# Kernel tuning notes

Measured on AMD Instinct MI355X. Metric: run time of the kernel, lower is better.

## Reference

```python
import jax, jax.numpy as jnp
import numpy as np

B, S, D = 1, 512, 2048
H, KVH, HD = 16, 16, 128          # heads, kv heads, head_dim = D // H
E, K, I = 64, 6, 1408             # routed experts, top_k, moe intermediate
NSH = 2
ISH = NSH * I                     # shared expert intermediate
EPS = 1e-6
THETA = 10000.0
SCALE = HD ** -0.5


def setup_inputs() -> dict:
    key = jax.random.key(0)
    ks = jax.random.split(key, 12)
    s = 0.02
    rn = lambda k, shape: s * jax.random.normal(k, shape, dtype=jnp.float32)
    return {
        "positions": jnp.arange(B * S, dtype=jnp.int32).reshape(B, S),
        "hidden_states": jax.random.normal(ks[0], (B, S, D), dtype=jnp.float32),
        "residual": jax.random.normal(ks[1], (B, S, D), dtype=jnp.float32),
        "ln1_w": jnp.ones((D,), jnp.float32),
        "ln2_w": jnp.ones((D,), jnp.float32),
        "wqkv": rn(ks[2], ((H + 2 * KVH) * HD, D)),
        "wo": rn(ks[3], (D, H * HD)),
        "gate_w": rn(ks[4], (E, D)),
        "w1": rn(ks[5], (E, 2 * I, D)),   # packed gate_up per expert
        "w2": rn(ks[6], (E, D, I)),       # down per expert
        "sw1": rn(ks[7], (2 * ISH, D)),   # shared expert gate_up
        "sw2": rn(ks[8], (D, ISH)),       # shared expert down
    }


def _rmsnorm(x, w):
    var = jnp.mean(x * x, axis=-1, keepdims=True)
    return x * jax.lax.rsqrt(var + EPS) * w


def _rope(x, pos):
    # x: [B, S, n_heads, HD], neox style (rotate halves), full rotary dim
    half = HD // 2
    inv_freq = 1.0 / (THETA ** (jnp.arange(half, dtype=jnp.float32) * 2.0 / HD))
    ang = pos.astype(jnp.float32)[..., None] * inv_freq        # [B, S, half]
    cos = jnp.cos(ang)[:, :, None, :]
    sin = jnp.sin(ang)[:, :, None, :]
    x1, x2 = jnp.split(x, 2, axis=-1)
    return jnp.concatenate([x1 * cos - x2 * sin, x2 * cos + x1 * sin], axis=-1)


def _swiglu(x, w_gate_up, w_down):
    gu = x @ w_gate_up.T
    g, u = jnp.split(gu, 2, axis=-1)
    return (jax.nn.silu(g) * u) @ w_down.T


def reference(positions, hidden_states, residual, ln1_w, ln2_w, wqkv, wo,
              gate_w, w1, w2, sw1, sw2):
    # --- input_layernorm with fused residual add (vLLM RMSNorm semantics) ---
    x = hidden_states + residual
    residual = x
    h = _rmsnorm(x, ln1_w)

    # --- attention: qkv proj, RoPE, causal attention (prefill), o proj ---
    qkv = h @ wqkv.T                                           # [B, S, (H+2KVH)*HD]
    q, k, v = jnp.split(qkv, [H * HD, (H + KVH) * HD], axis=-1)
    q = q.reshape(B, S, H, HD)
    k = k.reshape(B, S, KVH, HD)
    v = v.reshape(B, S, KVH, HD)
    q = _rope(q, positions)
    k = _rope(k, positions)
    scores = jnp.einsum("bqhd,bkhd->bhqk", q, k) * SCALE
    causal = jnp.tril(jnp.ones((S, S), dtype=bool))
    scores = jnp.where(causal, scores, -jnp.inf)
    attn = jax.nn.softmax(scores, axis=-1)
    ctx = jnp.einsum("bhqk,bkhd->bqhd", attn, v).reshape(B, S, H * HD)
    h = ctx @ wo.T

    # --- post_attention_layernorm with fused residual add ---
    x = h + residual
    residual = x
    h = _rmsnorm(x, ln2_w)

    # --- MoE: shared expert + softmax gate + top-k dispatch ---
    xt = h.reshape(B * S, D)                                   # [T, D]
    T = B * S
    shared = _swiglu(xt, sw1, sw2)                             # [T, D]
    logits = xt @ gate_w.T                                     # [T, E]
    probs = jax.nn.softmax(logits.astype(jnp.float32), axis=-1)
    topw, topi = jax.lax.top_k(probs, K)                       # [T, K]
    # norm_topk_prob = False -> no renormalization
    combine = jnp.zeros((T, E), jnp.float32).at[
        jnp.arange(T)[:, None], topi].add(topw)                # [T, E]

    def expert_step(acc, ew):
        w1e, w2e, ce = ew                                      # [2I,D], [D,I], [T]
        out = _swiglu(xt, w1e, w2e)                            # [T, D]
        return acc + ce[:, None] * out, None

    moe_out, _ = jax.lax.scan(expert_step, jnp.zeros_like(xt),
                              (w1, w2, combine.T))
    out = (moe_out + shared).reshape(B, S, D)
    return out, residual
```

## Files before the change

kernel.cpp:

```cpp
#include <hip/hip_runtime.h>
#include <hip/hip_bf16.h>


typedef __attribute__((ext_vector_type(4))) float  f32x4;
typedef __attribute__((ext_vector_type(8))) short  short8;
typedef __attribute__((ext_vector_type(8))) unsigned short ushort8;

#define SS    512
#define DD    2048
#define NH    16
#define HDIM  128
#define NQKV  6144
#define NEXP  64
#define TOPK  6
#define IEXP  1408
#define ISHE  2816
#define MAXTILE 128
#define ATT_SCALE 0.08838834764831845f

__device__ __forceinline__ float u2f(unsigned short u) {
  return __uint_as_float(((unsigned int)u) << 16);
}
__device__ __forceinline__ unsigned short f2u(float f) {
  __hip_bfloat16 h = __float2bfloat16(f);
  return *reinterpret_cast<unsigned short*>(&h);
}
__device__ __forceinline__ ushort8 cvt8(f32x4 a, f32x4 b) {
  ushort8 r;
  r[0]=f2u(a[0]); r[1]=f2u(a[1]); r[2]=f2u(a[2]); r[3]=f2u(a[3]);
  r[4]=f2u(b[0]); r[5]=f2u(b[1]); r[6]=f2u(b[2]); r[7]=f2u(b[3]);
  return r;
}

__global__ __launch_bounds__(256) void addnorm1_k(
    const float* __restrict__ hid, const float* __restrict__ res,
    const float* __restrict__ w, float* __restrict__ x1,
    unsigned short* __restrict__ h1)
{
  int t = blockIdx.x, tid = threadIdx.x;
  long long base = (long long)t * DD + tid * 8;
  float x[8]; float ss = 0.f;
#pragma unroll
  for (int i = 0; i < 8; i++) {
    x[i] = hid[base + i] + res[base + i];
    ss += x[i] * x[i]; x1[base + i] = x[i];
  }
#pragma unroll
  for (int o = 1; o < 64; o <<= 1) ss += __shfl_xor(ss, o);
  __shared__ float r4[4];
  if ((tid & 63) == 0) r4[tid >> 6] = ss;
  __syncthreads();
  ss = r4[0] + r4[1] + r4[2] + r4[3];
  float rr = rsqrtf(ss * (1.f / DD) + 1e-6f);
#pragma unroll
  for (int i = 0; i < 8; i++) h1[base + i] = f2u(x[i] * rr * w[tid * 8 + i]);
}

__global__ __launch_bounds__(256) void addnorm2_k(
    const unsigned short* __restrict__ attn, const float* __restrict__ x1,
    const float* __restrict__ w, float* __restrict__ resid_out,
    unsigned short* __restrict__ h3)
{
  int t = blockIdx.x, tid = threadIdx.x;
  long long base = (long long)t * DD + tid * 8;
  ushort8 va = *(const ushort8*)(attn + base);
  float x[8]; float ss = 0.f;
#pragma unroll
  for (int i = 0; i < 8; i++) {
    x[i] = u2f(va[i]) + x1[base + i]; ss += x[i] * x[i];
    resid_out[base + i] = x[i];
  }
#pragma unroll
  for (int o = 1; o < 64; o <<= 1) ss += __shfl_xor(ss, o);
  __shared__ float r4[4];
  if ((tid & 63) == 0) r4[tid >> 6] = ss;
  __syncthreads();
  ss = r4[0] + r4[1] + r4[2] + r4[3];
  float rr = rsqrtf(ss * (1.f / DD) + 1e-6f);
#pragma unroll
  for (int i = 0; i < 8; i++) h3[base + i] = f2u(x[i] * rr * w[tid * 8 + i]);
}

template<int BN>
__global__ __launch_bounds__(256) void gemm_dense(
    const unsigned short* __restrict__ A, const float* __restrict__ W,
    unsigned short* __restrict__ C, int Nh, int K, int lda, int Mdense)
{
  constexpr int WN  = BN / 2;
  constexpr int NF  = WN / 16;
  constexpr int TPR = 256 / BN;
  constexpr int FPT = BN / 4;
  constexpr int NV  = FPT / 4;
  __shared__ __align__(16) unsigned short As[64][72];
  __shared__ __align__(16) unsigned short Bg[BN][72];

  int m0 = blockIdx.y * 64, cnt = Mdense;
  int n0 = blockIdx.x * BN;
  int tid = threadIdx.x;
  int sr  = tid >> 2;
  int sce = (tid & 3) * 16;
  int sr2 = tid / TPR;
  int sc2 = (tid % TPR) * FPT;

  int am = m0 + sr; if (am >= cnt) am = cnt - 1;
  const unsigned short* ap = A + (long long)am * lda + sce;
  const float* gp = W + (long long)(n0 + sr2) * K + sc2;

  int lane = tid & 63, w = tid >> 6;
  int wm = (w >> 1) * 32, wn = (w & 1) * WN;
  int l15 = lane & 15, hi = lane >> 4;

  f32x4 acc[2][NF] = {};
  ushort8 ra0, ra1;
  f32x4 rg[NV];

  ra0 = *(const ushort8*)(ap);
  ra1 = *(const ushort8*)(ap + 8);
#pragma unroll
  for (int i = 0; i < NV; i++) rg[i] = *(const f32x4*)(gp + 4 * i);

  for (int k0 = 0; k0 < K; k0 += 64) {
    __syncthreads();
    *(ushort8*)&As[sr][sce]     = ra0;
    *(ushort8*)&As[sr][sce + 8] = ra1;
#pragma unroll
    for (int i = 0; i < NV / 2; i++)
      *(ushort8*)&Bg[sr2][sc2 + i * 8] = cvt8(rg[2 * i], rg[2 * i + 1]);
    __syncthreads();
    if (k0 + 64 < K) {
      ra0 = *(const ushort8*)(ap + k0 + 64);
      ra1 = *(const ushort8*)(ap + k0 + 72);
#pragma unroll
      for (int i = 0; i < NV; i++) rg[i] = *(const f32x4*)(gp + k0 + 64 + 4 * i);
    }
#pragma unroll
    for (int kk = 0; kk < 2; kk++) {
      int kc = kk * 32 + hi * 8;
      short8 fa[2], fg[NF];
#pragma unroll
      for (int f = 0; f < 2; f++) fa[f] = *(const short8*)&As[wm + f * 16 + l15][kc];
#pragma unroll
      for (int f = 0; f < NF; f++) fg[f] = *(const short8*)&Bg[wn + f * 16 + l15][kc];
#pragma unroll
      for (int fm = 0; fm < 2; fm++)
#pragma unroll
        for (int fn = 0; fn < NF; fn++)
          acc[fm][fn] = __builtin_amdgcn_mfma_f32_16x16x32_bf16(fa[fm], fg[fn], acc[fm][fn], 0, 0, 0);
    }
  }

  int r0q = hi * 4;
#pragma unroll
  for (int fm = 0; fm < 2; fm++) {
#pragma unroll
    for (int j = 0; j < 4; j++) {
      int m = m0 + wm + fm * 16 + r0q + j;
      if (m >= cnt) continue;
      unsigned short* Cp = C + (long long)m * Nh + n0 + wn;
#pragma unroll
      for (int fn = 0; fn < NF; fn++)
        Cp[fn * 16 + l15] = f2u(acc[fm][fn][j]);
    }
  }
}

template<int STAGE>
__global__ __launch_bounds__(256) void moe_k(
    const unsigned short* __restrict__ h3,
    const unsigned short* __restrict__ act_e_in, const unsigned short* __restrict__ act_sh_in,
    const float* __restrict__ w1, const float* __restrict__ sw1,
    const float* __restrict__ w2, const float* __restrict__ sw2,
    unsigned short* __restrict__ act_e_out, unsigned short* __restrict__ act_sh_out,
    unsigned short* __restrict__ out_e, unsigned short* __restrict__ shared_o,
    const int* __restrict__ e_cnt, const int* __restrict__ e_off,
    const int* __restrict__ tok_list, const float* __restrict__ wslot,
    const int* __restrict__ tile_tab, const int* __restrict__ ntiles)
{
  constexpr bool SILU = (STAGE == 0);
  __shared__ __align__(16) unsigned short As[64][72];
  __shared__ __align__(16) unsigned short Bg[64][72];
  __shared__ __align__(16) unsigned short Bu[SILU ? 64 : 1][72];

  int y = blockIdx.y;
  if (y >= *ntiles) return;
  int tt = tile_tab[y];
  int e = tt >> 8;
  int m0 = (tt & 255) * 64;
  bool sh = (e == NEXP);
  int cnt  = sh ? SS : e_cnt[e];
  int roff = sh ? 0 : e_off[e];
  int n0 = blockIdx.x * 64;

  int Nh, K, lda;
  const float* Wb;
  const unsigned short* Abase;
  unsigned short* Cb;
  if (STAGE == 0) {
    K = DD; lda = DD; Abase = h3;
    if (sh) { Nh = ISHE; Wb = sw1; Cb = act_sh_out; }
    else    { Nh = IEXP; Wb = w1 + (long long)e * 2 * IEXP * DD; Cb = act_e_out; }
    if (n0 >= Nh) return;
  } else {
    Nh = DD;
    if (sh) { K = ISHE; lda = ISHE; Abase = act_sh_in; Wb = sw2; Cb = shared_o; }
    else    { K = IEXP; lda = IEXP; Abase = act_e_in;
              Wb = w2 + (long long)e * DD * IEXP; Cb = out_e; }
  }

  int tid = threadIdx.x;
  int sr  = tid >> 2;
  int sce = (tid & 3) * 16;

  int am = m0 + sr; if (am >= cnt) am = cnt - 1;
  int arow;
  if (STAGE == 0) arow = sh ? am : tok_list[roff + am];
  else            arow = sh ? am : roff + am;
  const unsigned short* ap = Abase + (long long)arow * lda + sce;
  const float* gp = Wb + (long long)(n0 + sr) * K + sce;
  const float* up = SILU ? (Wb + (long long)(Nh + n0 + sr) * K + sce) : nullptr;

  int lane = tid & 63, wid = tid >> 6;
  int wm = (wid >> 1) * 32, wn = (wid & 1) * 32;
  int l15 = lane & 15, hi = lane >> 4;

  f32x4 acc[2][2] = {};
  f32x4 accU[2][2] = {};
  ushort8 raA0, raA1, raB0, raB1;
  f32x4 rgA[4], ruA[4], rgB[4], ruB[4];

#define MLOAD(k, r0, r1, g, u)                                     \
  do {                                                             \
    r0 = *(const ushort8*)(ap + (k));                              \
    r1 = *(const ushort8*)(ap + (k) + 8);                          \
    _Pragma("unroll")                                              \
    for (int i_ = 0; i_ < 4; i_++) g[i_] = *(const f32x4*)(gp + (k) + 4 * i_); \
    if (SILU) {                                                    \
      _Pragma("unroll")                                            \
      for (int i_ = 0; i_ < 4; i_++) u[i_] = *(const f32x4*)(up + (k) + 4 * i_); \
    }                                                              \
  } while (0)

#define MSTORE(r0, r1, g, u)                                       \
  do {                                                             \
    *(ushort8*)&As[sr][sce]     = r0;                              \
    *(ushort8*)&As[sr][sce + 8] = r1;                              \
    *(ushort8*)&Bg[sr][sce]     = cvt8(g[0], g[1]);                \
    *(ushort8*)&Bg[sr][sce + 8] = cvt8(g[2], g[3]);                \
    if (SILU) {                                                    \
      *(ushort8*)&Bu[sr][sce]     = cvt8(u[0], u[1]);              \
      *(ushort8*)&Bu[sr][sce + 8] = cvt8(u[2], u[3]);              \
    }                                                              \
  } while (0)

#define MMFMA                                                      \
  do {                                                             \
    _Pragma("unroll")                                              \
    for (int kk = 0; kk < 2; kk++) {                               \
      int kc = kk * 32 + hi * 8;                                   \
      short8 fa[2], fg[2];                                         \
      _Pragma("unroll")                                            \
      for (int f = 0; f < 2; f++) {                                \
        fa[f] = *(const short8*)&As[wm + f * 16 + l15][kc];        \
        fg[f] = *(const short8*)&Bg[wn + f * 16 + l15][kc];        \
      }                                                            \
      _Pragma("unroll")                                            \
      for (int fm = 0; fm < 2; fm++)                               \
        _Pragma("unroll")                                          \
        for (int fn = 0; fn < 2; fn++)                             \
          acc[fm][fn] = __builtin_amdgcn_mfma_f32_16x16x32_bf16(fa[fm], fg[fn], acc[fm][fn], 0, 0, 0); \
      if (SILU) {                                                  \
        short8 fu[2];                                              \
        _Pragma("unroll")                                          \
        for (int f = 0; f < 2; f++) fu[f] = *(const short8*)&Bu[wn + f * 16 + l15][kc]; \
        _Pragma("unroll")                                          \
        for (int fm = 0; fm < 2; fm++)                             \
          _Pragma("unroll")                                        \
          for (int fn = 0; fn < 2; fn++)                           \
            accU[fm][fn] = __builtin_amdgcn_mfma_f32_16x16x32_bf16(fa[fm], fu[fn], accU[fm][fn], 0, 0, 0); \
      }                                                            \
    }                                                              \
  } while (0)

  MLOAD(0,  raA0, raA1, rgA, ruA);
  MLOAD(64, raB0, raB1, rgB, ruB);
  for (int k0 = 0; k0 < K; k0 += 128) {
    __syncthreads();
    MSTORE(raA0, raA1, rgA, ruA);
    __syncthreads();
    if (k0 + 128 < K) MLOAD(k0 + 128, raA0, raA1, rgA, ruA);
    MMFMA;
    __syncthreads();
    MSTORE(raB0, raB1, rgB, ruB);
    __syncthreads();
    if (k0 + 192 < K) MLOAD(k0 + 192, raB0, raB1, rgB, ruB);
    MMFMA;
  }
#undef MLOAD
#undef MSTORE
#undef MMFMA

  int r0q = hi * 4;
#pragma unroll
  for (int fm = 0; fm < 2; fm++) {
#pragma unroll
    for (int j = 0; j < 4; j++) {
      int m = m0 + wm + fm * 16 + r0q + j;
      if (m >= cnt) continue;
      long long crow = sh ? m : (roff + m);
      float scale = (STAGE == 1 && !sh) ? wslot[crow] : 1.f;
      unsigned short* Cp = Cb + crow * (long long)Nh + n0 + wn;
#pragma unroll
      for (int fn = 0; fn < 2; fn++) {
        float v;
        if (SILU) {
          float g = acc[fm][fn][j], u = accU[fm][fn][j];
          v = (g / (1.f + __expf(-g))) * u;
        } else v = acc[fm][fn][j];
        Cp[fn * 16 + l15] = f2u(v * scale);
      }
    }
  }
}

__global__ __launch_bounds__(256) void rope_k(
    const int* __restrict__ pos, const unsigned short* __restrict__ qkv,
    unsigned short* __restrict__ qr, unsigned short* __restrict__ kr)
{
  int t = blockIdx.x, tid = threadIdx.x;
  __shared__ float cs[64], sn[64];
  if (tid < 64) {
    float inv = __expf(-((float)(2 * tid) / 128.f) * logf(10000.f));
    float ang = (float)pos[t] * inv;
    cs[tid] = cosf(ang); sn[tid] = sinf(ang);
  }
  __syncthreads();
  const unsigned short* row = qkv + (long long)t * NQKV;
  for (int idx = tid; idx < NH * 64; idx += 256) {
    int hh = idx >> 6, i = idx & 63;
    long long o = ((long long)hh * SS + t) * HDIM;
    float x1 = u2f(row[hh*128 + i]), x2 = u2f(row[hh*128 + i + 64]);
    qr[o + i]      = f2u(x1 * cs[i] - x2 * sn[i]);
    qr[o + i + 64] = f2u(x2 * cs[i] + x1 * sn[i]);
    float y1 = u2f(row[2048 + hh*128 + i]), y2 = u2f(row[2048 + hh*128 + i + 64]);
    kr[o + i]      = f2u(y1 * cs[i] - y2 * sn[i]);
    kr[o + i + 64] = f2u(y2 * cs[i] + y1 * sn[i]);
  }
}

__global__ __launch_bounds__(256) void attn_k(
    const unsigned short* __restrict__ qr, const unsigned short* __restrict__ kr,
    const unsigned short* __restrict__ qkv, unsigned short* __restrict__ ctx)
{
  int h = blockIdx.x, qt = blockIdx.y, q0 = qt * 64;
  int tid = threadIdx.x, lane = tid & 63, w = tid >> 6;
  int l15 = lane & 15, hi = lane >> 4;

  __shared__ unsigned short Vt[128][72];
  __shared__ unsigned short Pl[4][16][72];

  short8 qf[4];
  const unsigned short* Qb = qr + ((long long)h * SS + q0 + w * 16 + l15) * HDIM + hi * 8;
#pragma unroll
  for (int kf = 0; kf < 4; kf++) qf[kf] = *(const short8*)(Qb + kf * 32);

  f32x4 o[8] = {};
  float m_run[4] = {-1e30f, -1e30f, -1e30f, -1e30f};
  float l_run[4] = {};
  int myq = w * 16 + hi * 4;

  int ntile = qt + 1;
  for (int kt = 0; kt < ntile; kt++) {
    int kbase = kt * 64;
    __syncthreads();
    {
      int r = lane, d0 = w * 32;
      const unsigned short* Vp = qkv + (long long)(kbase + r) * NQKV + 4096 + h * HDIM + d0;
#pragma unroll
      for (int c = 0; c < 4; c++) {
        ushort8 v = *(const ushort8*)(Vp + c * 8);
#pragma unroll
        for (int i = 0; i < 8; i++) Vt[d0 + c * 8 + i][r] = v[i];
      }
    }
    f32x4 s[4] = {};
    const unsigned short* Kb = kr + ((long long)h * SS + kbase) * HDIM + hi * 8;
#pragma unroll
    for (int nf = 0; nf < 4; nf++) {
      const unsigned short* Kp = Kb + (long long)(nf * 16 + l15) * HDIM;
#pragma unroll
      for (int kf = 0; kf < 4; kf++) {
        short8 kf8 = *(const short8*)(Kp + kf * 32);
        s[nf] = __builtin_amdgcn_mfma_f32_16x16x32_bf16(qf[kf], kf8, s[nf], 0, 0, 0);
      }
    }
    bool diag = (kt == qt);
#pragma unroll
    for (int nf = 0; nf < 4; nf++) {
      int keyl = nf * 16 + l15;
#pragma unroll
      for (int j = 0; j < 4; j++) {
        float sv = s[nf][j] * ATT_SCALE;
        if (diag && keyl > myq + j) sv = -1e30f;
        s[nf][j] = sv;
      }
    }
    float corr[4], mnew[4];
#pragma unroll
    for (int j = 0; j < 4; j++) {
      float mv = fmaxf(fmaxf(s[0][j], s[1][j]), fmaxf(s[2][j], s[3][j]));
#pragma unroll
      for (int ox = 1; ox < 16; ox <<= 1) mv = fmaxf(mv, __shfl_xor(mv, ox));
      mnew[j] = fmaxf(m_run[j], mv);
      corr[j] = __expf(m_run[j] - mnew[j]);
      m_run[j] = mnew[j];
    }
#pragma unroll
    for (int nf8 = 0; nf8 < 8; nf8++)
#pragma unroll
      for (int j = 0; j < 4; j++) o[nf8][j] *= corr[j];
    float rs[4] = {};
#pragma unroll
    for (int nf = 0; nf < 4; nf++) {
#pragma unroll
      for (int j = 0; j < 4; j++) {
        float pv = __expf(s[nf][j] - mnew[j]);
        rs[j] += pv;
        Pl[w][hi * 4 + j][nf * 16 + l15] = f2u(pv);
      }
    }
#pragma unroll
    for (int j = 0; j < 4; j++) {
      float sv = rs[j];
#pragma unroll
      for (int ox = 1; ox < 16; ox <<= 1) sv += __shfl_xor(sv, ox);
      l_run[j] = l_run[j] * corr[j] + sv;
    }
    __syncthreads();
#pragma unroll
    for (int kf2 = 0; kf2 < 2; kf2++) {
      short8 pa = *(const short8*)&Pl[w][l15][kf2 * 32 + hi * 8];
#pragma unroll
      for (int nf8 = 0; nf8 < 8; nf8++) {
        short8 vb = *(const short8*)&Vt[nf8 * 16 + l15][kf2 * 32 + hi * 8];
        o[nf8] = __builtin_amdgcn_mfma_f32_16x16x32_bf16(pa, vb, o[nf8], 0, 0, 0);
      }
    }
  }
#pragma unroll
  for (int j = 0; j < 4; j++) {
    float inv = 1.f / l_run[j];
    long long t = q0 + myq + j;
    unsigned short* Cp = ctx + t * (long long)DD + h * HDIM;
#pragma unroll
    for (int nf8 = 0; nf8 < 8; nf8++)
      Cp[nf8 * 16 + l15] = f2u(o[nf8][j] * inv);
  }
}

__global__ __launch_bounds__(256) void gating_k(
    const unsigned short* __restrict__ h3, const float* __restrict__ gw,
    int* __restrict__ topi, float* __restrict__ topw)
{
  int b = blockIdx.x, tid = threadIdx.x;
  int e = tid & 63, g = tid >> 6;
  __shared__ float p[8][NEXP];
  const float* wr = gw + (long long)e * DD;
  int t0 = b * 8 + g * 2;
  const unsigned short* h0 = h3 + (long long)t0 * DD;
  const unsigned short* h1 = h0 + DD;
  float a0 = 0.f, a1 = 0.f;
  for (int k = 0; k < DD; k += 8) {
    f32x4 w0 = *(const f32x4*)(wr + k);
    f32x4 w1 = *(const f32x4*)(wr + k + 4);
    ushort8 x0 = *(const ushort8*)(h0 + k);
    ushort8 x1 = *(const ushort8*)(h1 + k);
    a0 += u2f(x0[0])*w0[0] + u2f(x0[1])*w0[1] + u2f(x0[2])*w0[2] + u2f(x0[3])*w0[3]
        + u2f(x0[4])*w1[0] + u2f(x0[5])*w1[1] + u2f(x0[6])*w1[2] + u2f(x0[7])*w1[3];
    a1 += u2f(x1[0])*w0[0] + u2f(x1[1])*w0[1] + u2f(x1[2])*w0[2] + u2f(x1[3])*w0[3]
        + u2f(x1[4])*w1[0] + u2f(x1[5])*w1[1] + u2f(x1[6])*w1[2] + u2f(x1[7])*w1[3];
  }
  p[g * 2][e] = a0; p[g * 2 + 1][e] = a1;
  __syncthreads();
  if (tid < 8) {
    int t = b * 8 + tid;
    float* pr = p[tid];
    float mx = -1e30f;
    for (int j = 0; j < NEXP; j++) mx = fmaxf(mx, pr[j]);
    float s = 0.f;
    for (int j = 0; j < NEXP; j++) { pr[j] = __expf(pr[j] - mx); s += pr[j]; }
    float invs = 1.f / s;
    for (int j = 0; j < NEXP; j++) pr[j] *= invs;
    for (int r = 0; r < TOPK; r++) {
      int bi = 0; float bv = -1.f;
      for (int j = 0; j < NEXP; j++) if (pr[j] > bv) { bv = pr[j]; bi = j; }
      topi[t * TOPK + r] = bi; topw[t * TOPK + r] = bv; pr[bi] = -2.f;
    }
  }
}

__global__ __launch_bounds__(256) void route_k(
    const int* __restrict__ topi, const float* __restrict__ topw,
    int* __restrict__ ecnt, int* __restrict__ eoff,
    int* __restrict__ tok_list, int* __restrict__ slotg,
    float* __restrict__ wslot, int* __restrict__ tile_tab,
    int* __restrict__ ntiles)
{
  __shared__ int ti[SS * TOPK];
  __shared__ int c4[NEXP][4];
  __shared__ int ctot[NEXP];
  __shared__ int offs[NEXP + 1];
  int tid = threadIdx.x;
  for (int i = tid; i < SS * TOPK; i += 256) ti[i] = topi[i];
  __syncthreads();
  int e = tid >> 2, q = tid & 3;
  const int QW = SS * TOPK / 4;
  int lo = q * QW, hiQ = lo + QW;
  int n = 0;
  for (int i = lo; i < hiQ; i++) n += (ti[i] == e);
  c4[e][q] = n;
  __syncthreads();
  if (q == 0) {
    int s = c4[e][0] + c4[e][1] + c4[e][2] + c4[e][3];
    ctot[e] = s; ecnt[e] = s;
  }
  __syncthreads();
  if (tid == 0) {
    offs[0] = 0;
    for (int k = 0; k < NEXP; k++) offs[k + 1] = offs[k] + ctot[k];
    int nt = 0;
    for (int k = 0; k < NEXP; k++)
      for (int mt = 0; mt * 64 < ctot[k]; mt++) tile_tab[nt++] = (k << 8) | mt;
    for (int mt = 0; mt < SS / 64; mt++) tile_tab[nt++] = (NEXP << 8) | mt;
    *ntiles = nt;
  }
  __syncthreads();
  if (q == 0) eoff[e] = offs[e];
  int idx = offs[e];
  for (int qq = 0; qq < q; qq++) idx += c4[e][qq];
  for (int i = lo; i < hiQ; i++)
    if (ti[i] == e) {
      tok_list[idx] = i / TOPK; slotg[i] = idx; wslot[idx] = topw[i]; idx++;
    }
}

__global__ __launch_bounds__(256) void combine_k(
    const unsigned short* __restrict__ shared_o, const unsigned short* __restrict__ out_e,
    const int* __restrict__ slotg, float* __restrict__ outp)
{
  int t = blockIdx.x, tid = threadIdx.x;
  int sl[TOPK];
#pragma unroll
  for (int j = 0; j < TOPK; j++) sl[j] = slotg[t * TOPK + j];
  long long d0 = (long long)t * DD + tid * 8;
  ushort8 sh = *(const ushort8*)(shared_o + d0);
  float a[8];
#pragma unroll
  for (int i = 0; i < 8; i++) a[i] = u2f(sh[i]);
#pragma unroll
  for (int j = 0; j < TOPK; j++) {
    ushort8 v = *(const ushort8*)(out_e + (long long)sl[j] * DD + tid * 8);
#pragma unroll
    for (int i = 0; i < 8; i++) a[i] += u2f(v[i]);
  }
#pragma unroll
  for (int i = 0; i < 8; i++) outp[d0 + i] = a[i];
}

extern "C" void kernel_launch(void* const* d_in, const int* in_sizes, int n_in,
                              void* d_out, int out_size, void* d_ws, size_t ws_size,
                              hipStream_t stream)
{
  (void)in_sizes; (void)n_in; (void)out_size; (void)ws_size;
  const int*   positions = (const int*)d_in[0];
  const float* hidden    = (const float*)d_in[1];
  const float* residual  = (const float*)d_in[2];
  const float* ln1_w     = (const float*)d_in[3];
  const float* ln2_w     = (const float*)d_in[4];
  const float* wqkv      = (const float*)d_in[5];
  const float* wo        = (const float*)d_in[6];
  const float* gate_w    = (const float*)d_in[7];
  const float* w1        = (const float*)d_in[8];
  const float* w2        = (const float*)d_in[9];
  const float* sw1       = (const float*)d_in[10];
  const float* sw2       = (const float*)d_in[11];

  float* outp      = (float*)d_out;
  float* resid_out = outp + (size_t)SS * DD;

  char* p = (char*)d_ws;
  auto alloc = [&](size_t b) { void* r = p; p += (b + 255) & ~(size_t)255; return r; };
  float*          x1       = (float*)alloc((size_t)SS * DD * 4);
  unsigned short* h1       = (unsigned short*)alloc((size_t)SS * DD * 2);
  unsigned short* qkv      = (unsigned short*)alloc((size_t)SS * NQKV * 2);
  unsigned short* qr       = (unsigned short*)alloc((size_t)SS * DD * 2);
  unsigned short* kr       = (unsigned short*)alloc((size_t)SS * DD * 2);
  unsigned short* ctx      = (unsigned short*)alloc((size_t)SS * DD * 2);
  unsigned short* attnout  = (unsigned short*)alloc((size_t)SS * DD * 2);
  unsigned short* h3       = (unsigned short*)alloc((size_t)SS * DD * 2);
  unsigned short* act_sh   = (unsigned short*)alloc((size_t)SS * ISHE * 2);
  unsigned short* shared_o = (unsigned short*)alloc((size_t)SS * DD * 2);
  unsigned short* act_e    = (unsigned short*)alloc((size_t)SS * TOPK * IEXP * 2);
  unsigned short* out_e    = (unsigned short*)alloc((size_t)SS * TOPK * DD * 2);
  int*            topi     = (int*)alloc(SS * TOPK * 4);
  float*          topw     = (float*)alloc(SS * TOPK * 4);
  int*            slotg    = (int*)alloc(SS * TOPK * 4);
  int*            tok_list = (int*)alloc(SS * TOPK * 4);
  float*          wslot    = (float*)alloc(SS * TOPK * 4);
  int*            ecnt     = (int*)alloc(NEXP * 4);
  int*            eoff     = (int*)alloc(NEXP * 4);
  int*            tile_tab = (int*)alloc(MAXTILE * 4);
  int*            ntiles   = (int*)alloc(4);

  addnorm1_k<<<SS, 256, 0, stream>>>(hidden, residual, ln1_w, x1, h1);
  gemm_dense<128><<<dim3(NQKV/128, SS/64), 256, 0, stream>>>(h1, wqkv, qkv, NQKV, DD, DD, SS);
  rope_k<<<SS, 256, 0, stream>>>(positions, qkv, qr, kr);
  attn_k<<<dim3(NH, SS/64), 256, 0, stream>>>(qr, kr, qkv, ctx);
  gemm_dense<64><<<dim3(DD/64, SS/64), 256, 0, stream>>>(ctx, wo, attnout, DD, DD, DD, SS);
  addnorm2_k<<<SS, 256, 0, stream>>>(attnout, x1, ln2_w, resid_out, h3);
  gating_k<<<SS/8, 256, 0, stream>>>(h3, gate_w, topi, topw);
  route_k<<<1, 256, 0, stream>>>(topi, topw, ecnt, eoff, tok_list, slotg, wslot,
                                 tile_tab, ntiles);
  moe_k<0><<<dim3(ISHE/64, MAXTILE), 256, 0, stream>>>(
      h3, nullptr, nullptr, w1, sw1, w2, sw2, act_e, act_sh, nullptr, nullptr,
      ecnt, eoff, tok_list, wslot, tile_tab, ntiles);
  moe_k<1><<<dim3(DD/64, MAXTILE), 256, 0, stream>>>(
      nullptr, act_e, act_sh, w1, sw1, w2, sw2, nullptr, nullptr, out_e, shared_o,
      ecnt, eoff, tok_list, wslot, tile_tab, ntiles);
  combine_k<<<SS, 256, 0, stream>>>(shared_o, out_e, slotg, outp);
}
```

Before: 866.5 us.

## Pre-convert dense weights to bf16 and use async LDS-loading double-buffered GEMM

Adds a separate pass that converts the fp32 QKV and output-projection weights to bf16 before the dense GEMMs. Those GEMMs are replaced by a 64x64 kernel that copies bf16 tiles straight from global memory into XOR-swizzled, double-buffered LDS using global_load_lds. The aim is to take the fp32 conversion out of the GEMM inner loop and overlap the next tile's loads with the current tile's MFMAs. In exchange it writes and rereads about 32 MB of bf16 weights every call, and the QKV GEMM moves from 128-wide to 64-wide tiles, which reduces reuse of the A operand.

```diff
diff --git a/kernel.cpp b/kernel.cpp
--- a/kernel.cpp
+++ b/kernel.cpp
@@ -32,6 +32,21 @@
   return r;
 }
 
+typedef __attribute__((address_space(3))) unsigned int lds_uint;
+typedef const __attribute__((address_space(1))) unsigned int ga_uint;
+__device__ __forceinline__ void gll16(const void* g, void* l) {
+  __builtin_amdgcn_global_load_lds((ga_uint*)g, (lds_uint*)l, 16, 0, 0);
+}
+
+__global__ __launch_bounds__(256) void cvtw_k(
+    const float* __restrict__ src, unsigned short* __restrict__ dst)
+{
+  long long i = ((long long)blockIdx.x * 256 + threadIdx.x) * 8;
+  f32x4 a = *(const f32x4*)(src + i);
+  f32x4 b = *(const f32x4*)(src + i + 4);
+  *(ushort8*)(dst + i) = cvt8(a, b);
+}
+
 __global__ __launch_bounds__(256) void addnorm1_k(
     const float* __restrict__ hid, const float* __restrict__ res,
     const float* __restrict__ w, float* __restrict__ x1,
@@ -81,73 +96,63 @@
   for (int i = 0; i < 8; i++) h3[base + i] = f2u(x[i] * rr * w[tid * 8 + i]);
 }
 
-template<int BN>
-__global__ __launch_bounds__(256) void gemm_dense(
-    const unsigned short* __restrict__ A, const float* __restrict__ W,
-    unsigned short* __restrict__ C, int Nh, int K, int lda, int Mdense)
-{
-  constexpr int WN  = BN / 2;
-  constexpr int NF  = WN / 16;
-  constexpr int TPR = 256 / BN;
-  constexpr int FPT = BN / 4;
-  constexpr int NV  = FPT / 4;
-  __shared__ __align__(16) unsigned short As[64][72];
-  __shared__ __align__(16) unsigned short Bg[BN][72];
-
-  int m0 = blockIdx.y * 64, cnt = Mdense;
-  int n0 = blockIdx.x * BN;
-  int tid = threadIdx.x;
-  int sr  = tid >> 2;
-  int sce = (tid & 3) * 16;
-  int sr2 = tid / TPR;
-  int sc2 = (tid % TPR) * FPT;
-
-  int am = m0 + sr; if (am >= cnt) am = cnt - 1;
-  const unsigned short* ap = A + (long long)am * lda + sce;
-  const float* gp = W + (long long)(n0 + sr2) * K + sc2;
-
-  int lane = tid & 63, w = tid >> 6;
-  int wm = (w >> 1) * 32, wn = (w & 1) * WN;
+__global__ __launch_bounds__(256) void gemm_bb(
+    const unsigned short* __restrict__ A, const unsigned short* __restrict__ W,
+    unsigned short* __restrict__ C, int Nh, int K, int lda)
+{
+  __shared__ __align__(16) unsigned short As[2][64][64];
+  __shared__ __align__(16) unsigned short Bs[2][64][64];
+
+  int m0 = blockIdx.y * 64;
+  int n0 = blockIdx.x * 64;
+  int tid = threadIdx.x, lane = tid & 63, w = tid >> 6;
+
+  const unsigned short* asrc[2];
+  const unsigned short* bsrc[2];
+#pragma unroll
+  for (int i = 0; i < 2; i++) {
+    int c = w + i * 4;
+    int r = c * 8 + (lane >> 3);
+    int col = ((lane & 7) ^ (lane >> 3)) << 3;
+    asrc[i] = A + (long long)(m0 + r) * lda + col;
+    bsrc[i] = W + (long long)(n0 + r) * K + col;
+  }
+
+  int wm = (w >> 1) * 32, wn = (w & 1) * 32;
   int l15 = lane & 15, hi = lane >> 4;
-
-  f32x4 acc[2][NF] = {};
-  ushort8 ra0, ra1;
-  f32x4 rg[NV];
-
-  ra0 = *(const ushort8*)(ap);
-  ra1 = *(const ushort8*)(ap + 8);
-#pragma unroll
-  for (int i = 0; i < NV; i++) rg[i] = *(const f32x4*)(gp + 4 * i);
-
-  for (int k0 = 0; k0 < K; k0 += 64) {
+  int key = l15 & 7;
+
+  f32x4 acc[2][2] = {};
+
+#define BSTAGE(buf, k0)                                                  \
+  do {                                                                   \
+    gll16((const char*)asrc[0] + (k0) * 2, &As[buf][w * 8][0]);          \
+    gll16((const char*)asrc[1] + (k0) * 2, &As[buf][(w + 4) * 8][0]);    \
+    gll16((const char*)bsrc[0] + (k0) * 2, &Bs[buf][w * 8][0]);          \
+    gll16((const char*)bsrc[1] + (k0) * 2, &Bs[buf][(w + 4) * 8][0]);    \
+  } while (0)
+
+  BSTAGE(0, 0);
+  int buf = 0;
+  for (int k0 = 0; k0 < K; k0 += 64, buf ^= 1) {
     __syncthreads();
-    *(ushort8*)&As[sr][sce]     = ra0;
-    *(ushort8*)&As[sr][sce + 8] = ra1;
-#pragma unroll
-    for (int i = 0; i < NV / 2; i++)
-      *(ushort8*)&Bg[sr2][sc2 + i * 8] = cvt8(rg[2 * i], rg[2 * i + 1]);
-    __syncthreads();
-    if (k0 + 64 < K) {
-      ra0 = *(const ushort8*)(ap + k0 + 64);
-      ra1 = *(const ushort8*)(ap + k0 + 72);
-#pragma unroll
-      for (int i = 0; i < NV; i++) rg[i] = *(const f32x4*)(gp + k0 + 64 + 4 * i);
-    }
+    if (k0 + 64 < K) BSTAGE(buf ^ 1, k0 + 64);
 #pragma unroll
     for (int kk = 0; kk < 2; kk++) {
-      int kc = kk * 32 + hi * 8;
-      short8 fa[2], fg[NF];
-#pragma unroll
-      for (int f = 0; f < 2; f++) fa[f] = *(const short8*)&As[wm + f * 16 + l15][kc];
-#pragma unroll
-      for (int f = 0; f < NF; f++) fg[f] = *(const short8*)&Bg[wn + f * 16 + l15][kc];
+      short8 fa[2], fb[2];
+#pragma unroll
+      for (int f = 0; f < 2; f++) {
+        fa[f] = *(const short8*)&As[buf][wm + f * 16 + l15][(((kk << 2) + hi) ^ key) << 3];
+        fb[f] = *(const short8*)&Bs[buf][wn + f * 16 + l15][(((kk << 2) + hi) ^ key) << 3];
+      }
 #pragma unroll
       for (int fm = 0; fm < 2; fm++)
 #pragma unroll
-        for (int fn = 0; fn < NF; fn++)
-          acc[fm][fn] = __builtin_amdgcn_mfma_f32_16x16x32_bf16(fa[fm], fg[fn], acc[fm][fn], 0, 0, 0);
-    }
-  }
+        for (int fn = 0; fn < 2; fn++)
+          acc[fm][fn] = __builtin_amdgcn_mfma_f32_16x16x32_bf16(fa[fm], fb[fn], acc[fm][fn], 0, 0, 0);
+    }
+  }
+#undef BSTAGE
 
   int r0q = hi * 4;
 #pragma unroll
@@ -155,10 +160,9 @@
 #pragma unroll
     for (int j = 0; j < 4; j++) {
       int m = m0 + wm + fm * 16 + r0q + j;
-      if (m >= cnt) continue;
       unsigned short* Cp = C + (long long)m * Nh + n0 + wn;
 #pragma unroll
-      for (int fn = 0; fn < NF; fn++)
+      for (int fn = 0; fn < 2; fn++)
         Cp[fn * 16 + l15] = f2u(acc[fm][fn][j]);
     }
   }
@@ -601,6 +605,8 @@
   unsigned short* shared_o = (unsigned short*)alloc((size_t)SS * DD * 2);
   unsigned short* act_e    = (unsigned short*)alloc((size_t)SS * TOPK * IEXP * 2);
   unsigned short* out_e    = (unsigned short*)alloc((size_t)SS * TOPK * DD * 2);
+  unsigned short* wqkv_bf  = (unsigned short*)alloc((size_t)NQKV * DD * 2);
+  unsigned short* wo_bf    = (unsigned short*)alloc((size_t)DD * DD * 2);
   int*            topi     = (int*)alloc(SS * TOPK * 4);
   float*          topw     = (float*)alloc(SS * TOPK * 4);
   int*            slotg    = (int*)alloc(SS * TOPK * 4);
@@ -611,11 +617,13 @@
   int*            tile_tab = (int*)alloc(MAXTILE * 4);
   int*            ntiles   = (int*)alloc(4);
 
+  cvtw_k<<<(NQKV * DD) / 2048, 256, 0, stream>>>(wqkv, wqkv_bf);
+  cvtw_k<<<(DD * DD) / 2048, 256, 0, stream>>>(wo, wo_bf);
   addnorm1_k<<<SS, 256, 0, stream>>>(hidden, residual, ln1_w, x1, h1);
-  gemm_dense<128><<<dim3(NQKV/128, SS/64), 256, 0, stream>>>(h1, wqkv, qkv, NQKV, DD, DD, SS);
+  gemm_bb<<<dim3(NQKV/64, SS/64), 256, 0, stream>>>(h1, wqkv_bf, qkv, NQKV, DD, DD);
   rope_k<<<SS, 256, 0, stream>>>(positions, qkv, qr, kr);
   attn_k<<<dim3(NH, SS/64), 256, 0, stream>>>(qr, kr, qkv, ctx);
-  gemm_dense<64><<<dim3(DD/64, SS/64), 256, 0, stream>>>(ctx, wo, attnout, DD, DD, DD, SS);
+  gemm_bb<<<dim3(DD/64, SS/64), 256, 0, stream>>>(ctx, wo_bf, attnout, DD, DD, DD);
   addnorm2_k<<<SS, 256, 0, stream>>>(attnout, x1, ln2_w, resid_out, h3);
   gating_k<<<SS/8, 256, 0, stream>>>(h3, gate_w, topi, topw);
   route_k<<<1, 256, 0, stream>>>(topi, topw, ecnt, eoff, tok_list, slotg, wslot,
```

Result: faster. 833.8 us (-3.8%).
